# Kernel tuning notes

Hardware: AMD Instinct MI355X
Metric: run time of the kernel (lower is better)

The kernel has to match this reference:

```python
import jax, jax.numpy as jnp
import numpy as np

HEADS = 8
DEPTH = 4
DIM = 128
FF_DIM = 4 * DIM
EPS = 1e-5


def _layer_norm(x, g, b):
    m = jnp.mean(x, axis=-1, keepdims=True)
    v = jnp.mean(jnp.square(x - m), axis=-1, keepdims=True)
    return (x - m) * jax.lax.rsqrt(v + EPS) * g + b


def _linear_attn(x, Wq, Wk, Wv, Wo, bo):
    # lucidrains linear-attention-transformer global (non-causal) linear attention
    b, n, d = x.shape
    dh = d // HEADS
    q = (x @ Wq).reshape(b, n, HEADS, dh).transpose(0, 2, 1, 3)  # bhnd
    k = (x @ Wk).reshape(b, n, HEADS, dh).transpose(0, 2, 1, 3)
    v = (x @ Wv).reshape(b, n, HEADS, dh).transpose(0, 2, 1, 3)
    q = jax.nn.softmax(q, axis=-1) * (dh ** -0.5)  # softmax over feature dim
    k = jax.nn.softmax(k, axis=2)                  # softmax over sequence dim
    ctx = jnp.einsum('bhnd,bhne->bhde', k, v)      # [b,h,dh,dh]
    o = jnp.einsum('bhnd,bhde->bhne', q, ctx)
    o = o.transpose(0, 2, 1, 3).reshape(b, n, d)
    return o @ Wo + bo


def _ff(x, W1, b1, W2, b2):
    return jax.nn.gelu(x @ W1 + b1) @ W2 + b2


def _stack(x, p):
    Wq, Wk, Wv, Wo, bo, g1, be1, g2, be2, W1, bf1, W2, bf2 = p
    for i in range(DEPTH):  # fixed small depth, structurally distinct params
        x = x + _linear_attn(_layer_norm(x, g1[i], be1[i]), Wq[i], Wk[i], Wv[i], Wo[i], bo[i])
        x = x + _ff(_layer_norm(x, g2[i], be2[i]), W1[i], bf1[i], W2[i], bf2[i])
    return x


def _make_stack_params(key):
    ks = jax.random.split(key, 6)
    w = lambda k, s: jax.random.normal(k, s, jnp.float32) * 0.02
    return dict(
        Wq=w(ks[0], (DEPTH, DIM, DIM)), Wk=w(ks[1], (DEPTH, DIM, DIM)),
        Wv=w(ks[2], (DEPTH, DIM, DIM)), Wo=w(ks[3], (DEPTH, DIM, DIM)),
        bo=jnp.zeros((DEPTH, DIM), jnp.float32),
        g1=jnp.ones((DEPTH, DIM), jnp.float32), be1=jnp.zeros((DEPTH, DIM), jnp.float32),
        g2=jnp.ones((DEPTH, DIM), jnp.float32), be2=jnp.zeros((DEPTH, DIM), jnp.float32),
        W1=w(ks[4], (DEPTH, DIM, FF_DIM)), bf1=jnp.zeros((DEPTH, FF_DIM), jnp.float32),
        W2=w(ks[5], (DEPTH, FF_DIM, DIM)), bf2=jnp.zeros((DEPTH, DIM), jnp.float32),
    )


def setup_inputs() -> dict:
    key = jax.random.key(0)
    kx, kc, kt = jax.random.split(key, 3)
    x = jax.random.normal(kx, (64, DIM, 62, 64), jnp.float32)  # [B, emb, num_chan, num_patch]
    pc = {k + '_c': v for k, v in _make_stack_params(kc).items()}
    pt = {k + '_t': v for k, v in _make_stack_params(kt).items()}
    return {'x': x, **pc, **pt}


def reference(x,
              Wq_c, Wk_c, Wv_c, Wo_c, bo_c, g1_c, be1_c, g2_c, be2_c, W1_c, bf1_c, W2_c, bf2_c,
              Wq_t, Wk_t, Wv_t, Wo_t, bo_t, g1_t, be1_t, g2_t, be2_t, W1_t, bf1_t, W2_t, bf2_t):
    b, e, c, p = x.shape
    h = jnp.transpose(x, (0, 3, 2, 1)).reshape(b * p, c, e)  # [B*P, C, E] channel attention
    h = _stack(h, (Wq_c, Wk_c, Wv_c, Wo_c, bo_c, g1_c, be1_c, g2_c, be2_c, W1_c, bf1_c, W2_c, bf2_c)).mean(1)
    h = h.reshape(b, p, e)                                   # [B, P, E] temporal attention
    h = _stack(h, (Wq_t, Wk_t, Wv_t, Wo_t, bo_t, g1_t, be1_t, g2_t, be2_t, W1_t, bf1_t, W2_t, bf2_t)).mean(1)
    return h
```

## Files before the change

### kernel.cpp

```cpp
#include <hip/hip_runtime.h>
#include <stdint.h>

typedef unsigned short u16;
typedef unsigned int   u32;
typedef __attribute__((ext_vector_type(8))) short short8;
typedef __attribute__((ext_vector_type(4))) float f32x4;

#define HEADS  8
#define DH     16
#define DIM    128
#define FFD    512
#define NDEPTH 4
#define NEPS   1e-5f
#define NT     256
#define NTP    256
#define LDA    136

#define U_N    14336
#define BK_OFF 2048
#define KT_OFF 2048
#define VT_OFF 10240

__device__ __forceinline__ float bf2f(u16 u) { return __uint_as_float(((u32)u) << 16); }
__device__ __forceinline__ u16 f2bf(float f) {
    u32 u = __float_as_uint(f);
    u32 r = (u + 0x7FFFu + ((u >> 16) & 1u)) >> 16;
    return (u16)r;
}

template <typename T> struct VT;
template <> struct VT<u16> {
    static __device__ __forceinline__ float ld(const u16* p) { return bf2f(*p); }
    static __device__ __forceinline__ void st(u16* p, float v) { *p = f2bf(v); }
};
template <> struct VT<float> {
    static __device__ __forceinline__ float ld(const float* p) { return *p; }
    static __device__ __forceinline__ void st(float* p, float v) { *p = v; }
};

struct SPv { const void* q[13]; };
struct WTs { const u16 *q, *k, *v, *o, *w1, *w2; };

template <typename T> struct SP {
    const T *bo, *g1, *be1, *g2, *be2, *bf1, *bf2;
    __device__ __forceinline__ SP(const SPv& s) {
        bo = (const T*)s.q[4];  g1 = (const T*)s.q[5];  be1 = (const T*)s.q[6];
        g2 = (const T*)s.q[7];  be2 = (const T*)s.q[8]; bf1 = (const T*)s.q[10];
        bf2 = (const T*)s.q[12];
    }
};

__device__ __forceinline__ void zero_acc(f32x4 acc[4][2]) {
    #pragma unroll
    for (int i = 0; i < 4; ++i)
        #pragma unroll
        for (int j = 0; j < 2; ++j) {
            acc[i][j].x = 0.f; acc[i][j].y = 0.f; acc[i][j].z = 0.f; acc[i][j].w = 0.f;
        }
}

__device__ __forceinline__ void gemm_lds(const u16* Ab, const u16* WT, int Ks,
                                         int nc0, int lane, f32x4 acc[4][2]) {
    const int n = lane & 15, quad = lane >> 4;
    #pragma unroll
    for (int ks = 0; ks < 4; ++ks) {
        short8 b0 = *(const short8*)(WT + (size_t)(nc0 + n) * Ks + ks * 32 + quad * 8);
        short8 b1 = *(const short8*)(WT + (size_t)(nc0 + 16 + n) * Ks + ks * 32 + quad * 8);
        #pragma unroll
        for (int mt = 0; mt < 4; ++mt) {
            short8 a = *(const short8*)(Ab + (mt * 16 + n) * LDA + ks * 32 + quad * 8);
            acc[mt][0] = __builtin_amdgcn_mfma_f32_16x16x32_bf16(a, b0, acc[mt][0], 0, 0, 0);
            acc[mt][1] = __builtin_amdgcn_mfma_f32_16x16x32_bf16(a, b1, acc[mt][1], 0, 0, 0);
        }
    }
}

__device__ __forceinline__ void store_bf16_tile(u16* dst, const f32x4 acc[4][2],
                                                int nc0, int lane) {
    const int c = lane & 15, quad = lane >> 4;
    #pragma unroll
    for (int mt = 0; mt < 4; ++mt)
        #pragma unroll
        for (int nt = 0; nt < 2; ++nt) {
            const float* a = (const float*)&acc[mt][nt];
            #pragma unroll
            for (int r = 0; r < 4; ++r)
                dst[(mt * 16 + quad * 4 + r) * LDA + nc0 + nt * 16 + c] = f2bf(a[r]);
        }
}

template <int MV, typename T>
__device__ __forceinline__ void ln_frag(const f32x4 (&h)[4][2], u16* yb, float* red,
                                        const T* g, const T* be,
                                        int lane, int quad, int nc0, int wn) {
    const int cid = lane & 15;
    const int col0 = nc0 + cid, col1 = col0 + 16;
    #pragma unroll
    for (int mt = 0; mt < 4; ++mt) {
        float s1[4], s2[4];
        #pragma unroll
        for (int r = 0; r < 4; ++r) {
            float a = h[mt][0][r], b = h[mt][1][r];
            s1[r] = a + b;
            s2[r] = fmaf(a, a, b * b);
        }
        #pragma unroll
        for (int m = 1; m <= 8; m <<= 1)
            #pragma unroll
            for (int r = 0; r < 4; ++r) {
                s1[r] += __shfl_xor(s1[r], m, 64);
                s2[r] += __shfl_xor(s2[r], m, 64);
            }
        if (cid == 0) {
            #pragma unroll
            for (int r = 0; r < 4; ++r) {
                const int row = mt * 16 + quad * 4 + r;
                red[row * 8 + wn]     = s1[r];
                red[row * 8 + 4 + wn] = s2[r];
            }
        }
    }
    __syncthreads();
    const float gl0 = VT<T>::ld(g + col0), gl1 = VT<T>::ld(g + col1);
    const float bl0 = VT<T>::ld(be + col0), bl1 = VT<T>::ld(be + col1);
    #pragma unroll
    for (int mt = 0; mt < 4; ++mt)
        #pragma unroll
        for (int r = 0; r < 4; ++r) {
            const int row = mt * 16 + quad * 4 + r;
            float4 p1 = *(const float4*)&red[row * 8];
            float4 p2 = *(const float4*)&red[row * 8 + 4];
            float t1 = (p1.x + p1.y) + (p1.z + p1.w);
            float t2 = (p2.x + p2.y) + (p2.z + p2.w);
            float mean = t1 * (1.0f / 128.0f);
            float var  = fmaxf(t2 * (1.0f / 128.0f) - mean * mean, 0.0f);
            float rstd = rsqrtf(var + NEPS);
            const bool valid = row < MV;
            float o0 = valid ? fmaf((h[mt][0][r] - mean) * rstd, gl0, bl0) : 0.0f;
            float o1 = valid ? fmaf((h[mt][1][r] - mean) * rstd, gl1, bl1) : 0.0f;
            yb[row * LDA + col0] = f2bf(o0);
            yb[row * LDA + col1] = f2bf(o1);
        }
    __syncthreads();
}

template <int MV>
__device__ __forceinline__ void ksoftmax_reg(f32x4 (&acc)[4][2], int lane) {
    const int quad = lane >> 4;
    #pragma unroll
    for (int nt = 0; nt < 2; ++nt) {
        float mx = -1e30f;
        #pragma unroll
        for (int mt = 0; mt < 4; ++mt)
            #pragma unroll
            for (int r = 0; r < 4; ++r) {
                const int lrow = mt * 16 + quad * 4 + r;
                mx = fmaxf(mx, (lrow < MV) ? acc[mt][nt][r] : -1e30f);
            }
        mx = fmaxf(mx, __shfl_xor(mx, 16, 64));
        mx = fmaxf(mx, __shfl_xor(mx, 32, 64));
        float s = 0.0f;
        #pragma unroll
        for (int mt = 0; mt < 4; ++mt)
            #pragma unroll
            for (int r = 0; r < 4; ++r) {
                const int lrow = mt * 16 + quad * 4 + r;
                float e = (lrow < MV) ? __expf(acc[mt][nt][r] - mx) : 0.0f;
                acc[mt][nt][r] = e;
                s += e;
            }
        s += __shfl_xor(s, 16, 64);
        s += __shfl_xor(s, 32, 64);
        const float inv = 1.0f / s;
        #pragma unroll
        for (int mt = 0; mt < 4; ++mt)
            #pragma unroll
            for (int r = 0; r < 4; ++r)
                acc[mt][nt][r] *= inv;
    }
}

__device__ __forceinline__ void qsoftmax_scale(f32x4 (&acc)[4][2], int lane) {
    (void)lane;
    #pragma unroll
    for (int mt = 0; mt < 4; ++mt)
        #pragma unroll
        for (int nt = 0; nt < 2; ++nt)
            #pragma unroll
            for (int r = 0; r < 4; ++r) {
                float v = acc[mt][nt][r];
                float mx = v;
                mx = fmaxf(mx, __shfl_xor(mx, 1, 64));
                mx = fmaxf(mx, __shfl_xor(mx, 2, 64));
                mx = fmaxf(mx, __shfl_xor(mx, 4, 64));
                mx = fmaxf(mx, __shfl_xor(mx, 8, 64));
                float e = __expf(v - mx);
                float s = e;
                s += __shfl_xor(s, 1, 64);
                s += __shfl_xor(s, 2, 64);
                s += __shfl_xor(s, 4, 64);
                s += __shfl_xor(s, 8, 64);
                acc[mt][nt][r] = e * (0.25f / s);
            }
}

__device__ __forceinline__ int swzk(int row, int n) {
    return ((row << 7) | (n << 1)) ^ ((row & 7) << 4);
}
__device__ __forceinline__ int swzb(int row, int n) {
    return ((row << 6) | (n << 1)) ^ ((row & 3) << 4);
}

template <int C>
__device__ __forceinline__ void store_kT_chunk(const f32x4 (&a)[4][2], u16* Th,
                                               int lane, int nc0) {
    const int cid = lane & 15, quad = lane >> 4;
    #pragma unroll
    for (int m = 0; m < 2; ++m)
        #pragma unroll
        for (int nt = 0; nt < 2; ++nt) {
            const int row = nc0 + nt * 16 + cid;
            #pragma unroll
            for (int rr = 0; rr < 2; ++rr) {
                const int n = C * 32 + m * 16 + quad * 4 + rr * 2;
                u32 w = (u32)f2bf(a[C * 2 + m][nt][rr * 2]) |
                        ((u32)f2bf(a[C * 2 + m][nt][rr * 2 + 1]) << 16);
                *(u32*)((char*)Th + swzk(row, n)) = w;
            }
        }
}

template <int C>
__device__ __forceinline__ void store_vT_chunk(const f32x4 (&a)[4][2], u16* Th,
                                               int lane, int nc0) {
    const int cid = lane & 15, quad = lane >> 4;
    #pragma unroll
    for (int m = 0; m < 2; ++m)
        #pragma unroll
        for (int nt = 0; nt < 2; ++nt) {
            const int row = nc0 + nt * 16 + cid;
            #pragma unroll
            for (int rr = 0; rr < 2; ++rr) {
                const int n = m * 16 + quad * 4 + rr * 2;
                u32 w = (u32)f2bf(a[C * 2 + m][nt][rr * 2]) |
                        ((u32)f2bf(a[C * 2 + m][nt][rr * 2 + 1]) << 16);
                *(u32*)((char*)Th + swzb(row, n)) = w;
            }
        }
}

template <int C>
__device__ __forceinline__ void ctx_chunk(const u16* kTs, const u16* vTs,
                                          f32x4 (&ctxacc)[2], int lane, int wn) {
    const int cid = lane & 15, quad = lane >> 4;
    #pragma unroll
    for (int h01 = 0; h01 < 2; ++h01) {
        const int row = (wn * 2 + h01) * 16 + cid;
        short8 a = *(const short8*)((const char*)vTs + swzb(row, quad * 8));
        short8 b = *(const short8*)((const char*)kTs + swzk(row, C * 32 + quad * 8));
        ctxacc[h01] = __builtin_amdgcn_mfma_f32_16x16x32_bf16(a, b, ctxacc[h01], 0, 0, 0);
    }
}

__device__ __forceinline__ void o_mfma(u16* qb, const u16* ctxs, int wn, int lane) {
    const int cid = lane & 15, quad = lane >> 4;
    f32x4 z; z.x = 0.f; z.y = 0.f; z.z = 0.f; z.w = 0.f;
    #pragma unroll
    for (int h01 = 0; h01 < 2; ++h01) {
        const int hd = wn * 2 + h01;
        short8 b = {0, 0, 0, 0, 0, 0, 0, 0};
        if (quad < 2)
            b = *(const short8*)(ctxs + hd * 256 + cid * 16 + quad * 8);
        #pragma unroll
        for (int mt = 0; mt < 4; ++mt) {
            short8 a = *(const short8*)(qb + (mt * 16 + cid) * LDA + hd * DH + (quad & 1) * 8);
            f32x4 o = __builtin_amdgcn_mfma_f32_16x16x32_bf16(a, b, z, 0, 0, 0);
            #pragma unroll
            for (int r = 0; r < 4; ++r)
                qb[(mt * 16 + quad * 4 + r) * LDA + hd * DH + cid] = f2bf(o[r]);
        }
    }
}

__device__ __forceinline__ float gelu_f(float v) {
    float u = 0.7978845608028654f * fmaf(0.044715f * v, v * v, v);
    u = fminf(fmaxf(u, -20.0f), 20.0f);
    float e  = __expf(2.0f * u);
    float th = 1.0f - 2.0f / (e + 1.0f);
    return 0.5f * v * (1.0f + th);
}

template <int MV, typename T>
__device__ __forceinline__ void run_stack(f32x4 (&h)[4][2], u16* yb, u16* U16,
                                          const WTs& wt, const SP<T>& p) {
    const int tid = threadIdx.x;
    const int lane = tid & 63, wn = tid >> 6;
    const int quad = lane >> 4, cid = lane & 15;
    const int nc0 = wn * 32;
    const int col0 = nc0 + cid, col1 = col0 + 16;
    float* red  = (float*)U16;
    u16*   bK   = U16 + BK_OFF;
    u16*   kTs  = U16 + KT_OFF;
    u16*   vTs  = U16 + VT_OFF;
    u16*   ctxs = U16;

    for (int L = 0; L < NDEPTH; ++L) {
        const u16* WqT = wt.q + L * 16384;
        const u16* WkT = wt.k + L * 16384;
        const u16* WvT = wt.v + L * 16384;
        const u16* WoT = wt.o + L * 16384;
        const u16* W1T = wt.w1 + L * 65536;
        const u16* W2T = wt.w2 + L * 65536;

        ln_frag<MV, T>(h, yb, red, p.g1 + L * DIM, p.be1 + L * DIM, lane, quad, nc0, wn);

        f32x4 acc[4][2];
        zero_acc(acc);
        gemm_lds(yb, WkT, DIM, nc0, lane, acc);
        ksoftmax_reg<MV>(acc, lane);
        store_kT_chunk<0>(acc, kTs, lane, nc0);
        store_kT_chunk<1>(acc, kTs, lane, nc0);
        zero_acc(acc);
        gemm_lds(yb, WvT, DIM, nc0, lane, acc);
        f32x4 ctxacc[2];
        #pragma unroll
        for (int i = 0; i < 2; ++i) {
            ctxacc[i].x = 0.f; ctxacc[i].y = 0.f; ctxacc[i].z = 0.f; ctxacc[i].w = 0.f;
        }
        store_vT_chunk<0>(acc, vTs, lane, nc0);
        ctx_chunk<0>(kTs, vTs, ctxacc, lane, wn);
        store_vT_chunk<1>(acc, vTs, lane, nc0);
        ctx_chunk<1>(kTs, vTs, ctxacc, lane, wn);
        #pragma unroll
        for (int h01 = 0; h01 < 2; ++h01)
            #pragma unroll
            for (int r = 0; r < 4; ++r)
                ctxs[(wn * 2 + h01) * 256 + (quad * 4 + r) * 16 + cid] = f2bf(ctxacc[h01][r]);

        zero_acc(acc);
        gemm_lds(yb, WqT, DIM, nc0, lane, acc);
        qsoftmax_scale(acc, lane);
        __syncthreads();
        store_bf16_tile(bK, acc, nc0, lane);
        o_mfma(bK, ctxs, wn, lane);
        __syncthreads();

        gemm_lds(bK, WoT, DIM, nc0, lane, h);
        {
            const float b0 = VT<T>::ld(p.bo + L * DIM + col0);
            const float b1 = VT<T>::ld(p.bo + L * DIM + col1);
            #pragma unroll
            for (int mt = 0; mt < 4; ++mt)
                #pragma unroll
                for (int r = 0; r < 4; ++r) { h[mt][0][r] += b0; h[mt][1][r] += b1; }
        }

        ln_frag<MV, T>(h, yb, red, p.g2 + L * DIM, p.be2 + L * DIM, lane, quad, nc0, wn);

        for (int cc = 0; cc < 4; ++cc) {
            zero_acc(acc);
            gemm_lds(yb, W1T + cc * 128 * DIM, DIM, nc0, lane, acc);
            const float b10 = VT<T>::ld(p.bf1 + L * FFD + cc * 128 + col0);
            const float b11 = VT<T>::ld(p.bf1 + L * FFD + cc * 128 + col1);
            #pragma unroll
            for (int mt = 0; mt < 4; ++mt)
                #pragma unroll
                for (int r = 0; r < 4; ++r) {
                    const int row = mt * 16 + quad * 4 + r;
                    bK[row * LDA + col0] = f2bf(gelu_f(acc[mt][0][r] + b10));
                    bK[row * LDA + col1] = f2bf(gelu_f(acc[mt][1][r] + b11));
                }
            __syncthreads();
            gemm_lds(bK, W2T + cc * 128, FFD, nc0, lane, h);
            if (cc < 3) __syncthreads();
        }
        {
            const float b0 = VT<T>::ld(p.bf2 + L * DIM + col0);
            const float b1 = VT<T>::ld(p.bf2 + L * DIM + col1);
            #pragma unroll
            for (int mt = 0; mt < 4; ++mt)
                #pragma unroll
                for (int r = 0; r < 4; ++r) { h[mt][0][r] += b0; h[mt][1][r] += b1; }
        }
    }
}

__device__ __forceinline__ bool is_bf16_g(const void* g1) {
    return *reinterpret_cast<const u32*>(g1) == 0x3F803F80u;
}

template <typename T>
__device__ __forceinline__ void channel_body(const T* x, const float* xT, int xmode,
                                             const SPv& pv, const WTs& wt,
                                             float* pooled, u16* yb, u16* U16) {
    SP<T> p(pv);
    const int tid = threadIdx.x;
    const int lane = tid & 63, wn = tid >> 6;
    const int quad = lane >> 4, cid = lane & 15;
    const int nc0 = wn * 32;
    const int col0 = nc0 + cid, col1 = col0 + 16;
    const int seq = blockIdx.x;

    f32x4 h[4][2];
    if (xmode) {
        const float* xrow = xT + (size_t)seq * 62 * DIM;
        #pragma unroll
        for (int mt = 0; mt < 4; ++mt)
            #pragma unroll
            for (int r = 0; r < 4; ++r) {
                const int row = mt * 16 + quad * 4 + r;
                h[mt][0][r] = (row < 62) ? xrow[row * DIM + col0] : 0.0f;
                h[mt][1][r] = (row < 62) ? xrow[row * DIM + col1] : 0.0f;
            }
    } else {
        const int b = seq >> 6, pp = seq & 63;
        #pragma unroll
        for (int mt = 0; mt < 4; ++mt)
            #pragma unroll
            for (int r = 0; r < 4; ++r) {
                const int row = mt * 16 + quad * 4 + r;
                h[mt][0][r] = (row < 62)
                    ? VT<T>::ld(x + (((size_t)b * DIM + col0) * 62 + row) * 64 + pp) : 0.0f;
                h[mt][1][r] = (row < 62)
                    ? VT<T>::ld(x + (((size_t)b * DIM + col1) * 62 + row) * 64 + pp) : 0.0f;
            }
    }

    run_stack<62, T>(h, yb, U16, wt, p);

    float s0 = 0.0f, s1 = 0.0f;
    #pragma unroll
    for (int mt = 0; mt < 4; ++mt)
        #pragma unroll
        for (int r = 0; r < 4; ++r) {
            const int row = mt * 16 + quad * 4 + r;
            if (row < 62) { s0 += h[mt][0][r]; s1 += h[mt][1][r]; }
        }
    s0 += __shfl_xor(s0, 16, 64); s0 += __shfl_xor(s0, 32, 64);
    s1 += __shfl_xor(s1, 16, 64); s1 += __shfl_xor(s1, 32, 64);
    if (quad == 0) {
        pooled[(size_t)seq * DIM + col0] = s0 * (1.0f / 62.0f);
        pooled[(size_t)seq * DIM + col1] = s1 * (1.0f / 62.0f);
    }
}

template <typename T>
__device__ __forceinline__ void temporal_body(const float* pooled, const SPv& pv,
                                              const WTs& wt, T* out, u16* yb, u16* U16) {
    SP<T> p(pv);
    const int tid = threadIdx.x;
    const int lane = tid & 63, wn = tid >> 6;
    const int quad = lane >> 4, cid = lane & 15;
    const int nc0 = wn * 32;
    const int col0 = nc0 + cid, col1 = col0 + 16;
    const int seq = blockIdx.x;

    f32x4 h[4][2];
    #pragma unroll
    for (int mt = 0; mt < 4; ++mt)
        #pragma unroll
        for (int r = 0; r < 4; ++r) {
            const int row = mt * 16 + quad * 4 + r;
            h[mt][0][r] = pooled[((size_t)seq * 64 + row) * DIM + col0];
            h[mt][1][r] = pooled[((size_t)seq * 64 + row) * DIM + col1];
        }

    run_stack<64, T>(h, yb, U16, wt, p);

    float s0 = 0.0f, s1 = 0.0f;
    #pragma unroll
    for (int mt = 0; mt < 4; ++mt)
        #pragma unroll
        for (int r = 0; r < 4; ++r) { s0 += h[mt][0][r]; s1 += h[mt][1][r]; }
    s0 += __shfl_xor(s0, 16, 64); s0 += __shfl_xor(s0, 32, 64);
    s1 += __shfl_xor(s1, 16, 64); s1 += __shfl_xor(s1, 32, 64);
    if (quad == 0) {
        VT<T>::st(out + (size_t)seq * DIM + col0, s0 * (1.0f / 64.0f));
        VT<T>::st(out + (size_t)seq * DIM + col1, s1 * (1.0f / 64.0f));
    }
}

__global__ __launch_bounds__(NT, 2) void k_channel(const void* xv, const float* xT,
                                                   int xmode, SPv pv, WTs wt,
                                                   float* __restrict__ pooled) {
    __shared__ __attribute__((aligned(16))) u16 yb[64 * LDA];
    __shared__ __attribute__((aligned(16))) u16 Ubuf[U_N];

    if (is_bf16_g(pv.q[5]))
        channel_body<u16>((const u16*)xv, xT, xmode, pv, wt, pooled, yb, Ubuf);
    else
        channel_body<float>((const float*)xv, xT, xmode, pv, wt, pooled, yb, Ubuf);
}

__global__ __launch_bounds__(NT, 2) void k_temporal(const float* __restrict__ pooled,
                                                    SPv pv, WTs wt, void* outv) {
    __shared__ __attribute__((aligned(16))) u16 yb[64 * LDA];
    __shared__ __attribute__((aligned(16))) u16 Ubuf[U_N];

    if (is_bf16_g(pv.q[5]))
        temporal_body<u16>(pooled, pv, wt, (u16*)outv, yb, Ubuf);
    else
        temporal_body<float>(pooled, pv, wt, (float*)outv, yb, Ubuf);
}

template <typename T>
__device__ __forceinline__ void prepx_body(const T* x, float* xT, float* t) {
    const int tid = threadIdx.x;
    const int b = blockIdx.x >> 3, cg = blockIdx.x & 7;
    const int c1 = (cg == 7) ? 62 : (cg * 8 + 8);
    for (int c = cg * 8; c < c1; ++c) {
        #pragma unroll 4
        for (int rep = 0; rep < 32; ++rep) {
            const int idx = rep * NTP + tid;
            const int e = idx >> 6, pp = idx & 63;
            t[pp * 132 + e] = VT<T>::ld(x + (((size_t)b * DIM + e) * 62 + c) * 64 + pp);
        }
        __syncthreads();
        #pragma unroll 4
        for (int rep = 0; rep < 32; ++rep) {
            const int idx = rep * NTP + tid;
            const int pp = idx >> 7, e = idx & 127;
            xT[((size_t)(b * 64 + pp) * 62 + c) * DIM + e] = t[pp * 132 + e];
        }
        __syncthreads();
    }
}

__global__ __launch_bounds__(NTP) void k_prepx(const void* xv, const void* g1, float* xT) {
    __shared__ float t[64 * 132];
    if (is_bf16_g(g1)) prepx_body<u16>((const u16*)xv, xT, t);
    else               prepx_body<float>((const float*)xv, xT, t);
}

struct TD { const void* src; u16* dst; int K; int N; int nelem; };
struct TDs { TD a[12]; const void* g1; };

__global__ __launch_bounds__(NTP) void k_prep(TDs t) {
    const bool bf = (*(const u32*)t.g1 == 0x3F803F80u);
    int idx = blockIdx.x * NTP + threadIdx.x;
    #pragma unroll 1
    for (int i = 0; i < 12; ++i) {
        if (idx < t.a[i].nelem) {
            const int K = t.a[i].K, N = t.a[i].N;
            const int l = idx / (K * N);
            const int r = idx - l * K * N;
            const int n = r / K;
            const int k = r - n * K;
            const size_t si = ((size_t)l * K + k) * N + n;
            float v = bf ? bf2f(((const u16*)t.a[i].src)[si])
                         : ((const float*)t.a[i].src)[si];
            t.a[i].dst[idx] = f2bf(v);
            return;
        }
        idx -= t.a[i].nelem;
    }
}

extern "C" void kernel_launch(void* const* d_in, const int* in_sizes, int n_in,
                              void* d_out, int out_size, void* d_ws, size_t ws_size,
                              hipStream_t stream) {
    (void)in_sizes; (void)n_in; (void)out_size;
    SPv pc, pt;
    for (int i = 0; i < 13; ++i) pc.q[i] = d_in[1 + i];
    for (int i = 0; i < 13; ++i) pt.q[i] = d_in[14 + i];

    float* pooled = (float*)d_ws;
    u16*   wtb    = (u16*)((char*)d_ws + (size_t)4096 * 128 * 4);
    const size_t XT_OFF = 8u << 20;
    float* xT     = (float*)((char*)d_ws + XT_OFF);
    const size_t xt_need = XT_OFF + (size_t)4096 * 62 * DIM * 4;
    const int xmode = (ws_size >= xt_need) ? 1 : 0;

    const int SQ = 4 * DIM * DIM;
    const int SF = 4 * DIM * FFD;
    const int STK = 4 * SQ + 2 * SF;

    WTs wc { wtb, wtb + SQ, wtb + 2 * SQ, wtb + 3 * SQ, wtb + 4 * SQ, wtb + 4 * SQ + SF };
    u16* wtb2 = wtb + STK;
    WTs wt2 { wtb2, wtb2 + SQ, wtb2 + 2 * SQ, wtb2 + 3 * SQ, wtb2 + 4 * SQ, wtb2 + 4 * SQ + SF };

    TDs td;
    td.a[0]  = { d_in[1],  (u16*)wc.q,  DIM, DIM, SQ };
    td.a[1]  = { d_in[2],  (u16*)wc.k,  DIM, DIM, SQ };
    td.a[2]  = { d_in[3],  (u16*)wc.v,  DIM, DIM, SQ };
    td.a[3]  = { d_in[4],  (u16*)wc.o,  DIM, DIM, SQ };
    td.a[4]  = { d_in[10], (u16*)wc.w1, DIM, FFD, SF };
    td.a[5]  = { d_in[12], (u16*)wc.w2, FFD, DIM, SF };
    td.a[6]  = { d_in[14], (u16*)wt2.q,  DIM, DIM, SQ };
    td.a[7]  = { d_in[15], (u16*)wt2.k,  DIM, DIM, SQ };
    td.a[8]  = { d_in[16], (u16*)wt2.v,  DIM, DIM, SQ };
    td.a[9]  = { d_in[17], (u16*)wt2.o,  DIM, DIM, SQ };
    td.a[10] = { d_in[23], (u16*)wt2.w1, DIM, FFD, SF };
    td.a[11] = { d_in[25], (u16*)wt2.w2, FFD, DIM, SF };
    td.g1 = d_in[6];

    const int total = 2 * STK;
    k_prep<<<dim3((total + NTP - 1) / NTP), dim3(NTP), 0, stream>>>(td);
    if (xmode)
        k_prepx<<<dim3(64 * 8), dim3(NTP), 0, stream>>>(d_in[0], d_in[6], xT);

    k_channel<<<dim3(4096), dim3(NT), 0, stream>>>(d_in[0], xT, xmode, pc, wc, pooled);
    k_temporal<<<dim3(64),  dim3(NT), 0, stream>>>(pooled, pt, wt2, d_out);
}
```

Measured before the change: 2.038 ms.

## Use 8 waves per block with one head per wave instead of 4 waves

Blocks grow from 256 to 512 threads, so each wave owns 16 output columns (one attention head) instead of 32. The GEMM, softmax, LayerNorm reduction and context computation are reworked so each wave handles one head, with per-wave transposed K/V scratch and a wider cross-wave reduction buffer. This aims to raise the number of active waves and cut per-thread register pressure. In exchange each B-fragment load feeds fewer MFMAs, shared memory per block grows, and barriers now synchronise twice as many waves.

```diff
diff --git a/kernel.cpp b/kernel.cpp
--- a/kernel.cpp
+++ b/kernel.cpp
@@ -12,11 +12,11 @@
 #define FFD    512
 #define NDEPTH 4
 #define NEPS   1e-5f
-#define NT     256
+#define NT     512
 #define NTP    256
 #define LDA    136
 
-#define U_N    14336
+#define U_N    18432
 #define BK_OFF 2048
 #define KT_OFF 2048
 #define VT_OFF 10240
@@ -50,59 +50,50 @@
     }
 };
 
-__device__ __forceinline__ void zero_acc(f32x4 acc[4][2]) {
-    #pragma unroll
-    for (int i = 0; i < 4; ++i)
-        #pragma unroll
-        for (int j = 0; j < 2; ++j) {
-            acc[i][j].x = 0.f; acc[i][j].y = 0.f; acc[i][j].z = 0.f; acc[i][j].w = 0.f;
-        }
+__device__ __forceinline__ void zero4(f32x4 acc[4]) {
+    #pragma unroll
+    for (int i = 0; i < 4; ++i) {
+        acc[i].x = 0.f; acc[i].y = 0.f; acc[i].z = 0.f; acc[i].w = 0.f;
+    }
 }
 
 __device__ __forceinline__ void gemm_lds(const u16* Ab, const u16* WT, int Ks,
-                                         int nc0, int lane, f32x4 acc[4][2]) {
+                                         int nc0, int lane, f32x4 acc[4]) {
     const int n = lane & 15, quad = lane >> 4;
     #pragma unroll
     for (int ks = 0; ks < 4; ++ks) {
         short8 b0 = *(const short8*)(WT + (size_t)(nc0 + n) * Ks + ks * 32 + quad * 8);
-        short8 b1 = *(const short8*)(WT + (size_t)(nc0 + 16 + n) * Ks + ks * 32 + quad * 8);
         #pragma unroll
         for (int mt = 0; mt < 4; ++mt) {
             short8 a = *(const short8*)(Ab + (mt * 16 + n) * LDA + ks * 32 + quad * 8);
-            acc[mt][0] = __builtin_amdgcn_mfma_f32_16x16x32_bf16(a, b0, acc[mt][0], 0, 0, 0);
-            acc[mt][1] = __builtin_amdgcn_mfma_f32_16x16x32_bf16(a, b1, acc[mt][1], 0, 0, 0);
-        }
-    }
-}
-
-__device__ __forceinline__ void store_bf16_tile(u16* dst, const f32x4 acc[4][2],
+            acc[mt] = __builtin_amdgcn_mfma_f32_16x16x32_bf16(a, b0, acc[mt], 0, 0, 0);
+        }
+    }
+}
+
+__device__ __forceinline__ void store_bf16_tile(u16* dst, const f32x4 acc[4],
                                                 int nc0, int lane) {
     const int c = lane & 15, quad = lane >> 4;
     #pragma unroll
     for (int mt = 0; mt < 4; ++mt)
         #pragma unroll
-        for (int nt = 0; nt < 2; ++nt) {
-            const float* a = (const float*)&acc[mt][nt];
-            #pragma unroll
-            for (int r = 0; r < 4; ++r)
-                dst[(mt * 16 + quad * 4 + r) * LDA + nc0 + nt * 16 + c] = f2bf(a[r]);
-        }
+        for (int r = 0; r < 4; ++r)
+            dst[(mt * 16 + quad * 4 + r) * LDA + nc0 + c] = f2bf(acc[mt][r]);
 }
 
 template <int MV, typename T>
-__device__ __forceinline__ void ln_frag(const f32x4 (&h)[4][2], u16* yb, float* red,
+__device__ __forceinline__ void ln_frag(const f32x4 (&h)[4], u16* yb, float* red,
                                         const T* g, const T* be,
-                                        int lane, int quad, int nc0, int wn) {
+                                        int lane, int quad, int col0, int wn) {
     const int cid = lane & 15;
-    const int col0 = nc0 + cid, col1 = col0 + 16;
     #pragma unroll
     for (int mt = 0; mt < 4; ++mt) {
         float s1[4], s2[4];
         #pragma unroll
         for (int r = 0; r < 4; ++r) {
-            float a = h[mt][0][r], b = h[mt][1][r];
-            s1[r] = a + b;
-            s2[r] = fmaf(a, a, b * b);
+            float a = h[mt][r];
+            s1[r] = a;
+            s2[r] = a * a;
         }
         #pragma unroll
         for (int m = 1; m <= 8; m <<= 1)
@@ -115,170 +106,127 @@
             #pragma unroll
             for (int r = 0; r < 4; ++r) {
                 const int row = mt * 16 + quad * 4 + r;
-                red[row * 8 + wn]     = s1[r];
-                red[row * 8 + 4 + wn] = s2[r];
+                red[row * 16 + wn]     = s1[r];
+                red[row * 16 + 8 + wn] = s2[r];
             }
         }
     }
     __syncthreads();
-    const float gl0 = VT<T>::ld(g + col0), gl1 = VT<T>::ld(g + col1);
-    const float bl0 = VT<T>::ld(be + col0), bl1 = VT<T>::ld(be + col1);
+    const float gl0 = VT<T>::ld(g + col0);
+    const float bl0 = VT<T>::ld(be + col0);
     #pragma unroll
     for (int mt = 0; mt < 4; ++mt)
         #pragma unroll
         for (int r = 0; r < 4; ++r) {
             const int row = mt * 16 + quad * 4 + r;
-            float4 p1 = *(const float4*)&red[row * 8];
-            float4 p2 = *(const float4*)&red[row * 8 + 4];
-            float t1 = (p1.x + p1.y) + (p1.z + p1.w);
-            float t2 = (p2.x + p2.y) + (p2.z + p2.w);
+            float4 a1 = *(const float4*)&red[row * 16];
+            float4 b1 = *(const float4*)&red[row * 16 + 4];
+            float4 a2 = *(const float4*)&red[row * 16 + 8];
+            float4 b2 = *(const float4*)&red[row * 16 + 12];
+            float t1 = ((a1.x + a1.y) + (a1.z + a1.w)) + ((b1.x + b1.y) + (b1.z + b1.w));
+            float t2 = ((a2.x + a2.y) + (a2.z + a2.w)) + ((b2.x + b2.y) + (b2.z + b2.w));
             float mean = t1 * (1.0f / 128.0f);
             float var  = fmaxf(t2 * (1.0f / 128.0f) - mean * mean, 0.0f);
             float rstd = rsqrtf(var + NEPS);
             const bool valid = row < MV;
-            float o0 = valid ? fmaf((h[mt][0][r] - mean) * rstd, gl0, bl0) : 0.0f;
-            float o1 = valid ? fmaf((h[mt][1][r] - mean) * rstd, gl1, bl1) : 0.0f;
+            float o0 = valid ? fmaf((h[mt][r] - mean) * rstd, gl0, bl0) : 0.0f;
             yb[row * LDA + col0] = f2bf(o0);
-            yb[row * LDA + col1] = f2bf(o1);
         }
     __syncthreads();
 }
 
 template <int MV>
-__device__ __forceinline__ void ksoftmax_reg(f32x4 (&acc)[4][2], int lane) {
+__device__ __forceinline__ void ksoftmax_reg(f32x4 (&acc)[4], int lane) {
     const int quad = lane >> 4;
-    #pragma unroll
-    for (int nt = 0; nt < 2; ++nt) {
-        float mx = -1e30f;
-        #pragma unroll
-        for (int mt = 0; mt < 4; ++mt)
-            #pragma unroll
-            for (int r = 0; r < 4; ++r) {
-                const int lrow = mt * 16 + quad * 4 + r;
-                mx = fmaxf(mx, (lrow < MV) ? acc[mt][nt][r] : -1e30f);
-            }
-        mx = fmaxf(mx, __shfl_xor(mx, 16, 64));
-        mx = fmaxf(mx, __shfl_xor(mx, 32, 64));
-        float s = 0.0f;
-        #pragma unroll
-        for (int mt = 0; mt < 4; ++mt)
-            #pragma unroll
-            for (int r = 0; r < 4; ++r) {
-                const int lrow = mt * 16 + quad * 4 + r;
-                float e = (lrow < MV) ? __expf(acc[mt][nt][r] - mx) : 0.0f;
-                acc[mt][nt][r] = e;
-                s += e;
-            }
-        s += __shfl_xor(s, 16, 64);
-        s += __shfl_xor(s, 32, 64);
-        const float inv = 1.0f / s;
-        #pragma unroll
-        for (int mt = 0; mt < 4; ++mt)
-            #pragma unroll
-            for (int r = 0; r < 4; ++r)
-                acc[mt][nt][r] *= inv;
-    }
-}
-
-__device__ __forceinline__ void qsoftmax_scale(f32x4 (&acc)[4][2], int lane) {
-    (void)lane;
-    #pragma unroll
-    for (int mt = 0; mt < 4; ++mt)
-        #pragma unroll
-        for (int nt = 0; nt < 2; ++nt)
-            #pragma unroll
-            for (int r = 0; r < 4; ++r) {
-                float v = acc[mt][nt][r];
-                float mx = v;
-                mx = fmaxf(mx, __shfl_xor(mx, 1, 64));
-                mx = fmaxf(mx, __shfl_xor(mx, 2, 64));
-                mx = fmaxf(mx, __shfl_xor(mx, 4, 64));
-                mx = fmaxf(mx, __shfl_xor(mx, 8, 64));
-                float e = __expf(v - mx);
-                float s = e;
-                s += __shfl_xor(s, 1, 64);
-                s += __shfl_xor(s, 2, 64);
-                s += __shfl_xor(s, 4, 64);
-                s += __shfl_xor(s, 8, 64);
-                acc[mt][nt][r] = e * (0.25f / s);
-            }
-}
-
-__device__ __forceinline__ int swzk(int row, int n) {
-    return ((row << 7) | (n << 1)) ^ ((row & 7) << 4);
-}
-__device__ __forceinline__ int swzb(int row, int n) {
-    return ((row << 6) | (n << 1)) ^ ((row & 3) << 4);
-}
-
-template <int C>
-__device__ __forceinline__ void store_kT_chunk(const f32x4 (&a)[4][2], u16* Th,
-                                               int lane, int nc0) {
+    float mx = -1e30f;
+    #pragma unroll
+    for (int mt = 0; mt < 4; ++mt)
+        #pragma unroll
+        for (int r = 0; r < 4; ++r) {
+            const int lrow = mt * 16 + quad * 4 + r;
+            mx = fmaxf(mx, (lrow < MV) ? acc[mt][r] : -1e30f);
+        }
+    mx = fmaxf(mx, __shfl_xor(mx, 16, 64));
+    mx = fmaxf(mx, __shfl_xor(mx, 32, 64));
+    float s = 0.0f;
+    #pragma unroll
+    for (int mt = 0; mt < 4; ++mt)
+        #pragma unroll
+        for (int r = 0; r < 4; ++r) {
+            const int lrow = mt * 16 + quad * 4 + r;
+            float e = (lrow < MV) ? __expf(acc[mt][r] - mx) : 0.0f;
+            acc[mt][r] = e;
+            s += e;
+        }
+    s += __shfl_xor(s, 16, 64);
+    s += __shfl_xor(s, 32, 64);
+    const float inv = 1.0f / s;
+    #pragma unroll
+    for (int mt = 0; mt < 4; ++mt)
+        #pragma unroll
+        for (int r = 0; r < 4; ++r)
+            acc[mt][r] *= inv;
+}
+
+__device__ __forceinline__ void qsoftmax_scale(f32x4 (&acc)[4]) {
+    #pragma unroll
+    for (int mt = 0; mt < 4; ++mt)
+        #pragma unroll
+        for (int r = 0; r < 4; ++r) {
+            float v = acc[mt][r];
+            float mx = v;
+            mx = fmaxf(mx, __shfl_xor(mx, 1, 64));
+            mx = fmaxf(mx, __shfl_xor(mx, 2, 64));
+            mx = fmaxf(mx, __shfl_xor(mx, 4, 64));
+            mx = fmaxf(mx, __shfl_xor(mx, 8, 64));
+            float e = __expf(v - mx);
+            float s = e;
+            s += __shfl_xor(s, 1, 64);
+            s += __shfl_xor(s, 2, 64);
+            s += __shfl_xor(s, 4, 64);
+            s += __shfl_xor(s, 8, 64);
+            acc[mt][r] = e * (0.25f / s);
+        }
+}
+
+__device__ __forceinline__ void store_T16(const f32x4 (&a)[4], u16* Tw, int lane) {
     const int cid = lane & 15, quad = lane >> 4;
     #pragma unroll
-    for (int m = 0; m < 2; ++m)
-        #pragma unroll
-        for (int nt = 0; nt < 2; ++nt) {
-            const int row = nc0 + nt * 16 + cid;
-            #pragma unroll
-            for (int rr = 0; rr < 2; ++rr) {
-                const int n = C * 32 + m * 16 + quad * 4 + rr * 2;
-                u32 w = (u32)f2bf(a[C * 2 + m][nt][rr * 2]) |
-                        ((u32)f2bf(a[C * 2 + m][nt][rr * 2 + 1]) << 16);
-                *(u32*)((char*)Th + swzk(row, n)) = w;
-            }
-        }
-}
-
-template <int C>
-__device__ __forceinline__ void store_vT_chunk(const f32x4 (&a)[4][2], u16* Th,
-                                               int lane, int nc0) {
+    for (int mt = 0; mt < 4; ++mt)
+        #pragma unroll
+        for (int rr = 0; rr < 2; ++rr) {
+            const int n = mt * 16 + quad * 4 + rr * 2;
+            u32 w = (u32)f2bf(a[mt][rr * 2]) | ((u32)f2bf(a[mt][rr * 2 + 1]) << 16);
+            int off = ((cid << 7) + (n << 1)) ^ ((cid & 7) << 4);
+            *(u32*)((char*)Tw + off) = w;
+        }
+}
+
+__device__ __forceinline__ void ctx16(const u16* kTw, const u16* vTw,
+                                      f32x4& ctxacc, int lane) {
     const int cid = lane & 15, quad = lane >> 4;
     #pragma unroll
-    for (int m = 0; m < 2; ++m)
-        #pragma unroll
-        for (int nt = 0; nt < 2; ++nt) {
-            const int row = nc0 + nt * 16 + cid;
-            #pragma unroll
-            for (int rr = 0; rr < 2; ++rr) {
-                const int n = m * 16 + quad * 4 + rr * 2;
-                u32 w = (u32)f2bf(a[C * 2 + m][nt][rr * 2]) |
-                        ((u32)f2bf(a[C * 2 + m][nt][rr * 2 + 1]) << 16);
-                *(u32*)((char*)Th + swzb(row, n)) = w;
-            }
-        }
-}
-
-template <int C>
-__device__ __forceinline__ void ctx_chunk(const u16* kTs, const u16* vTs,
-                                          f32x4 (&ctxacc)[2], int lane, int wn) {
-    const int cid = lane & 15, quad = lane >> 4;
-    #pragma unroll
-    for (int h01 = 0; h01 < 2; ++h01) {
-        const int row = (wn * 2 + h01) * 16 + cid;
-        short8 a = *(const short8*)((const char*)vTs + swzb(row, quad * 8));
-        short8 b = *(const short8*)((const char*)kTs + swzk(row, C * 32 + quad * 8));
-        ctxacc[h01] = __builtin_amdgcn_mfma_f32_16x16x32_bf16(a, b, ctxacc[h01], 0, 0, 0);
-    }
-}
-
-__device__ __forceinline__ void o_mfma(u16* qb, const u16* ctxs, int wn, int lane) {
+    for (int ks = 0; ks < 2; ++ks) {
+        int off = ((cid << 7) + ks * 64 + quad * 16) ^ ((cid & 7) << 4);
+        short8 a = *(const short8*)((const char*)vTw + off);
+        short8 b = *(const short8*)((const char*)kTw + off);
+        ctxacc = __builtin_amdgcn_mfma_f32_16x16x32_bf16(a, b, ctxacc, 0, 0, 0);
+    }
+}
+
+__device__ __forceinline__ void o_mfma16(u16* qb, const u16* ctxs, int wn, int lane) {
     const int cid = lane & 15, quad = lane >> 4;
     f32x4 z; z.x = 0.f; z.y = 0.f; z.z = 0.f; z.w = 0.f;
-    #pragma unroll
-    for (int h01 = 0; h01 < 2; ++h01) {
-        const int hd = wn * 2 + h01;
-        short8 b = {0, 0, 0, 0, 0, 0, 0, 0};
-        if (quad < 2)
-            b = *(const short8*)(ctxs + hd * 256 + cid * 16 + quad * 8);
-        #pragma unroll
-        for (int mt = 0; mt < 4; ++mt) {
-            short8 a = *(const short8*)(qb + (mt * 16 + cid) * LDA + hd * DH + (quad & 1) * 8);
-            f32x4 o = __builtin_amdgcn_mfma_f32_16x16x32_bf16(a, b, z, 0, 0, 0);
-            #pragma unroll
-            for (int r = 0; r < 4; ++r)
-                qb[(mt * 16 + quad * 4 + r) * LDA + hd * DH + cid] = f2bf(o[r]);
-        }
+    short8 b = {0, 0, 0, 0, 0, 0, 0, 0};
+    if (quad < 2)
+        b = *(const short8*)(ctxs + wn * 256 + cid * 16 + quad * 8);
+    #pragma unroll
+    for (int mt = 0; mt < 4; ++mt) {
+        short8 a = *(const short8*)(qb + (mt * 16 + cid) * LDA + wn * 16 + (quad & 1) * 8);
+        f32x4 o = __builtin_amdgcn_mfma_f32_16x16x32_bf16(a, b, z, 0, 0, 0);
+        #pragma unroll
+        for (int r = 0; r < 4; ++r)
+            qb[(mt * 16 + quad * 4 + r) * LDA + wn * 16 + cid] = f2bf(o[r]);
     }
 }
 
@@ -291,18 +239,18 @@
 }
 
 template <int MV, typename T>
-__device__ __forceinline__ void run_stack(f32x4 (&h)[4][2], u16* yb, u16* U16,
+__device__ __forceinline__ void run_stack(f32x4 (&h)[4], u16* yb, u16* U16,
                                           const WTs& wt, const SP<T>& p) {
     const int tid = threadIdx.x;
     const int lane = tid & 63, wn = tid >> 6;
     const int quad = lane >> 4, cid = lane & 15;
-    const int nc0 = wn * 32;
-    const int col0 = nc0 + cid, col1 = col0 + 16;
+    const int nc0 = wn * 16;
+    const int col0 = nc0 + cid;
     float* red  = (float*)U16;
+    u16*   ctxs = U16;
     u16*   bK   = U16 + BK_OFF;
-    u16*   kTs  = U16 + KT_OFF;
-    u16*   vTs  = U16 + VT_OFF;
-    u16*   ctxs = U16;
+    u16*   kTw  = U16 + KT_OFF + wn * 1024;
+    u16*   vTw  = U16 + VT_OFF + wn * 1024;
 
     for (int L = 0; L < NDEPTH; ++L) {
         const u16* WqT = wt.q + L * 16384;
@@ -312,63 +260,51 @@
         const u16* W1T = wt.w1 + L * 65536;
         const u16* W2T = wt.w2 + L * 65536;
 
-        ln_frag<MV, T>(h, yb, red, p.g1 + L * DIM, p.be1 + L * DIM, lane, quad, nc0, wn);
-
-        f32x4 acc[4][2];
-        zero_acc(acc);
+        ln_frag<MV, T>(h, yb, red, p.g1 + L * DIM, p.be1 + L * DIM, lane, quad, col0, wn);
+
+        f32x4 acc[4];
+        zero4(acc);
         gemm_lds(yb, WkT, DIM, nc0, lane, acc);
         ksoftmax_reg<MV>(acc, lane);
-        store_kT_chunk<0>(acc, kTs, lane, nc0);
-        store_kT_chunk<1>(acc, kTs, lane, nc0);
-        zero_acc(acc);
+        store_T16(acc, kTw, lane);
+        zero4(acc);
         gemm_lds(yb, WvT, DIM, nc0, lane, acc);
-        f32x4 ctxacc[2];
-        #pragma unroll
-        for (int i = 0; i < 2; ++i) {
-            ctxacc[i].x = 0.f; ctxacc[i].y = 0.f; ctxacc[i].z = 0.f; ctxacc[i].w = 0.f;
-        }
-        store_vT_chunk<0>(acc, vTs, lane, nc0);
-        ctx_chunk<0>(kTs, vTs, ctxacc, lane, wn);
-        store_vT_chunk<1>(acc, vTs, lane, nc0);
-        ctx_chunk<1>(kTs, vTs, ctxacc, lane, wn);
-        #pragma unroll
-        for (int h01 = 0; h01 < 2; ++h01)
-            #pragma unroll
-            for (int r = 0; r < 4; ++r)
-                ctxs[(wn * 2 + h01) * 256 + (quad * 4 + r) * 16 + cid] = f2bf(ctxacc[h01][r]);
-
-        zero_acc(acc);
+        store_T16(acc, vTw, lane);
+        f32x4 ctxacc; ctxacc.x = 0.f; ctxacc.y = 0.f; ctxacc.z = 0.f; ctxacc.w = 0.f;
+        ctx16(kTw, vTw, ctxacc, lane);
+        #pragma unroll
+        for (int r = 0; r < 4; ++r)
+            ctxs[wn * 256 + (quad * 4 + r) * 16 + cid] = f2bf(ctxacc[r]);
+
+        zero4(acc);
         gemm_lds(yb, WqT, DIM, nc0, lane, acc);
-        qsoftmax_scale(acc, lane);
+        qsoftmax_scale(acc);
         __syncthreads();
         store_bf16_tile(bK, acc, nc0, lane);
-        o_mfma(bK, ctxs, wn, lane);
+        o_mfma16(bK, ctxs, wn, lane);
         __syncthreads();
 
         gemm_lds(bK, WoT, DIM, nc0, lane, h);
         {
             const float b0 = VT<T>::ld(p.bo + L * DIM + col0);
-            const float b1 = VT<T>::ld(p.bo + L * DIM + col1);
             #pragma unroll
             for (int mt = 0; mt < 4; ++mt)
                 #pragma unroll
-                for (int r = 0; r < 4; ++r) { h[mt][0][r] += b0; h[mt][1][r] += b1; }
-        }
-
-        ln_frag<MV, T>(h, yb, red, p.g2 + L * DIM, p.be2 + L * DIM, lane, quad, nc0, wn);
+                for (int r = 0; r < 4; ++r) h[mt][r] += b0;
+        }
+
+        ln_frag<MV, T>(h, yb, red, p.g2 + L * DIM, p.be2 + L * DIM, lane, quad, col0, wn);
 
         for (int cc = 0; cc < 4; ++cc) {
-            zero_acc(acc);
+            zero4(acc);
             gemm_lds(yb, W1T + cc * 128 * DIM, DIM, nc0, lane, acc);
             const float b10 = VT<T>::ld(p.bf1 + L * FFD + cc * 128 + col0);
-            const float b11 = VT<T>::ld(p.bf1 + L * FFD + cc * 128 + col1);
             #pragma unroll
             for (int mt = 0; mt < 4; ++mt)
                 #pragma unroll
                 for (int r = 0; r < 4; ++r) {
                     const int row = mt * 16 + quad * 4 + r;
-                    bK[row * LDA + col0] = f2bf(gelu_f(acc[mt][0][r] + b10));
-                    bK[row * LDA + col1] = f2bf(gelu_f(acc[mt][1][r] + b11));
+                    bK[row * LDA + col0] = f2bf(gelu_f(acc[mt][r] + b10));
                 }
             __syncthreads();
             gemm_lds(bK, W2T + cc * 128, FFD, nc0, lane, h);
@@ -376,11 +312,10 @@
         }
         {
             const float b0 = VT<T>::ld(p.bf2 + L * DIM + col0);
-            const float b1 = VT<T>::ld(p.bf2 + L * DIM + col1);
             #pragma unroll
             for (int mt = 0; mt < 4; ++mt)
                 #pragma unroll
-                for (int r = 0; r < 4; ++r) { h[mt][0][r] += b0; h[mt][1][r] += b1; }
+                for (int r = 0; r < 4; ++r) h[mt][r] += b0;
         }
     }
 }
@@ -397,11 +332,10 @@
     const int tid = threadIdx.x;
     const int lane = tid & 63, wn = tid >> 6;
     const int quad = lane >> 4, cid = lane & 15;
-    const int nc0 = wn * 32;
-    const int col0 = nc0 + cid, col1 = col0 + 16;
+    const int col0 = wn * 16 + cid;
     const int seq = blockIdx.x;
 
-    f32x4 h[4][2];
+    f32x4 h[4];
     if (xmode) {
         const float* xrow = xT + (size_t)seq * 62 * DIM;
         #pragma unroll
@@ -409,8 +343,7 @@
             #pragma unroll
             for (int r = 0; r < 4; ++r) {
                 const int row = mt * 16 + quad * 4 + r;
-                h[mt][0][r] = (row < 62) ? xrow[row * DIM + col0] : 0.0f;
-                h[mt][1][r] = (row < 62) ? xrow[row * DIM + col1] : 0.0f;
+                h[mt][r] = (row < 62) ? xrow[row * DIM + col0] : 0.0f;
             }
     } else {
         const int b = seq >> 6, pp = seq & 63;
@@ -419,29 +352,24 @@
             #pragma unroll
             for (int r = 0; r < 4; ++r) {
                 const int row = mt * 16 + quad * 4 + r;
-                h[mt][0][r] = (row < 62)
+                h[mt][r] = (row < 62)
                     ? VT<T>::ld(x + (((size_t)b * DIM + col0) * 62 + row) * 64 + pp) : 0.0f;
-                h[mt][1][r] = (row < 62)
-                    ? VT<T>::ld(x + (((size_t)b * DIM + col1) * 62 + row) * 64 + pp) : 0.0f;
             }
     }
 
     run_stack<62, T>(h, yb, U16, wt, p);
 
-    float s0 = 0.0f, s1 = 0.0f;
+    float s0 = 0.0f;
     #pragma unroll
     for (int mt = 0; mt < 4; ++mt)
         #pragma unroll
         for (int r = 0; r < 4; ++r) {
             const int row = mt * 16 + quad * 4 + r;
-            if (row < 62) { s0 += h[mt][0][r]; s1 += h[mt][1][r]; }
+            if (row < 62) s0 += h[mt][r];
         }
     s0 += __shfl_xor(s0, 16, 64); s0 += __shfl_xor(s0, 32, 64);
-    s1 += __shfl_xor(s1, 16, 64); s1 += __shfl_xor(s1, 32, 64);
-    if (quad == 0) {
+    if (quad == 0)
         pooled[(size_t)seq * DIM + col0] = s0 * (1.0f / 62.0f);
-        pooled[(size_t)seq * DIM + col1] = s1 * (1.0f / 62.0f);
-    }
 }
 
 template <typename T>
@@ -451,36 +379,31 @@
     const int tid = threadIdx.x;
     const int lane = tid & 63, wn = tid >> 6;
     const int quad = lane >> 4, cid = lane & 15;
-    const int nc0 = wn * 32;
-    const int col0 = nc0 + cid, col1 = col0 + 16;
+    const int col0 = wn * 16 + cid;
     const int seq = blockIdx.x;
 
-    f32x4 h[4][2];
+    f32x4 h[4];
     #pragma unroll
     for (int mt = 0; mt < 4; ++mt)
         #pragma unroll
         for (int r = 0; r < 4; ++r) {
             const int row = mt * 16 + quad * 4 + r;
-            h[mt][0][r] = pooled[((size_t)seq * 64 + row) * DIM + col0];
-            h[mt][1][r] = pooled[((size_t)seq * 64 + row) * DIM + col1];
+            h[mt][r] = pooled[((size_t)seq * 64 + row) * DIM + col0];
         }
 
     run_stack<64, T>(h, yb, U16, wt, p);
 
-    float s0 = 0.0f, s1 = 0.0f;
-    #pragma unroll
-    for (int mt = 0; mt < 4; ++mt)
-        #pragma unroll
-        for (int r = 0; r < 4; ++r) { s0 += h[mt][0][r]; s1 += h[mt][1][r]; }
+    float s0 = 0.0f;
+    #pragma unroll
+    for (int mt = 0; mt < 4; ++mt)
+        #pragma unroll
+        for (int r = 0; r < 4; ++r) s0 += h[mt][r];
     s0 += __shfl_xor(s0, 16, 64); s0 += __shfl_xor(s0, 32, 64);
-    s1 += __shfl_xor(s1, 16, 64); s1 += __shfl_xor(s1, 32, 64);
-    if (quad == 0) {
+    if (quad == 0)
         VT<T>::st(out + (size_t)seq * DIM + col0, s0 * (1.0f / 64.0f));
-        VT<T>::st(out + (size_t)seq * DIM + col1, s1 * (1.0f / 64.0f));
-    }
-}
-
-__global__ __launch_bounds__(NT, 2) void k_channel(const void* xv, const float* xT,
+}
+
+__global__ __launch_bounds__(NT, 4) void k_channel(const void* xv, const float* xT,
                                                    int xmode, SPv pv, WTs wt,
                                                    float* __restrict__ pooled) {
     __shared__ __attribute__((aligned(16))) u16 yb[64 * LDA];
@@ -492,7 +415,7 @@
         channel_body<float>((const float*)xv, xT, xmode, pv, wt, pooled, yb, Ubuf);
 }
 
-__global__ __launch_bounds__(NT, 2) void k_temporal(const float* __restrict__ pooled,
+__global__ __launch_bounds__(NT, 4) void k_temporal(const float* __restrict__ pooled,
                                                     SPv pv, WTs wt, void* outv) {
     __shared__ __attribute__((aligned(16))) u16 yb[64 * LDA];
     __shared__ __attribute__((aligned(16))) u16 Ubuf[U_N];
```

Result: slower. 2.589 ms (+27.1%).

## Double-buffer FF hidden chunks in LDS and use fast reciprocals in softmax/GELU

Applied to the files above, without the earlier changes.

The feed-forward loop now ping-pongs between two LDS buffers. The next chunk's W1 GEMM and GELU are computed while the current chunk feeds the W2 GEMM, which removes one barrier per chunk. Divisions in the key softmax, query softmax and GELU are replaced with the hardware approximate reciprocal. The query softmax also drops its max-subtraction, which saves four shuffles per element but risks overflow for large logits. The LDS footprint grows by about 17 KB, which may lower occupancy.

```diff
diff --git a/kernel.cpp b/kernel.cpp
--- a/kernel.cpp
+++ b/kernel.cpp
@@ -16,10 +16,11 @@
 #define NTP    256
 #define LDA    136
 
-#define U_N    14336
-#define BK_OFF 2048
-#define KT_OFF 2048
-#define VT_OFF 10240
+#define U_N     23040
+#define BK_OFF  2048
+#define KT_OFF  2048
+#define VT_OFF  10240
+#define BK2_OFF 14336
 
 __device__ __forceinline__ float bf2f(u16 u) { return __uint_as_float(((u32)u) << 16); }
 __device__ __forceinline__ u16 f2bf(float f) {
@@ -171,7 +172,7 @@
             }
         s += __shfl_xor(s, 16, 64);
         s += __shfl_xor(s, 32, 64);
-        const float inv = 1.0f / s;
+        const float inv = __builtin_amdgcn_rcpf(s);
         #pragma unroll
         for (int mt = 0; mt < 4; ++mt)
             #pragma unroll
@@ -188,19 +189,13 @@
         for (int nt = 0; nt < 2; ++nt)
             #pragma unroll
             for (int r = 0; r < 4; ++r) {
-                float v = acc[mt][nt][r];
-                float mx = v;
-                mx = fmaxf(mx, __shfl_xor(mx, 1, 64));
-                mx = fmaxf(mx, __shfl_xor(mx, 2, 64));
-                mx = fmaxf(mx, __shfl_xor(mx, 4, 64));
-                mx = fmaxf(mx, __shfl_xor(mx, 8, 64));
-                float e = __expf(v - mx);
+                float e = __expf(acc[mt][nt][r]);
                 float s = e;
                 s += __shfl_xor(s, 1, 64);
                 s += __shfl_xor(s, 2, 64);
                 s += __shfl_xor(s, 4, 64);
                 s += __shfl_xor(s, 8, 64);
-                acc[mt][nt][r] = e * (0.25f / s);
+                acc[mt][nt][r] = e * (0.25f * __builtin_amdgcn_rcpf(s));
             }
 }
 
@@ -286,8 +281,24 @@
     float u = 0.7978845608028654f * fmaf(0.044715f * v, v * v, v);
     u = fminf(fmaxf(u, -20.0f), 20.0f);
     float e  = __expf(2.0f * u);
-    float th = 1.0f - 2.0f / (e + 1.0f);
+    float th = 1.0f - 2.0f * __builtin_amdgcn_rcpf(e + 1.0f);
     return 0.5f * v * (1.0f + th);
+}
+
+template <typename T>
+__device__ __forceinline__ void gelu_store(const f32x4 (&acc)[4][2], u16* dst,
+                                           const T* bf1, int col0, int col1,
+                                           int quad) {
+    const float b10 = VT<T>::ld(bf1 + col0);
+    const float b11 = VT<T>::ld(bf1 + col1);
+    #pragma unroll
+    for (int mt = 0; mt < 4; ++mt)
+        #pragma unroll
+        for (int r = 0; r < 4; ++r) {
+            const int row = mt * 16 + quad * 4 + r;
+            dst[row * LDA + col0] = f2bf(gelu_f(acc[mt][0][r] + b10));
+            dst[row * LDA + col1] = f2bf(gelu_f(acc[mt][1][r] + b11));
+        }
 }
 
 template <int MV, typename T>
@@ -299,7 +310,8 @@
     const int nc0 = wn * 32;
     const int col0 = nc0 + cid, col1 = col0 + 16;
     float* red  = (float*)U16;
-    u16*   bK   = U16 + BK_OFF;
+    u16*   bKa  = U16 + BK_OFF;
+    u16*   bKb  = U16 + BK2_OFF;
     u16*   kTs  = U16 + KT_OFF;
     u16*   vTs  = U16 + VT_OFF;
     u16*   ctxs = U16;
@@ -341,11 +353,11 @@
         gemm_lds(yb, WqT, DIM, nc0, lane, acc);
         qsoftmax_scale(acc, lane);
         __syncthreads();
-        store_bf16_tile(bK, acc, nc0, lane);
-        o_mfma(bK, ctxs, wn, lane);
+        store_bf16_tile(bKa, acc, nc0, lane);
+        o_mfma(bKa, ctxs, wn, lane);
         __syncthreads();
 
-        gemm_lds(bK, WoT, DIM, nc0, lane, h);
+        gemm_lds(bKa, WoT, DIM, nc0, lane, h);
         {
             const float b0 = VT<T>::ld(p.bo + L * DIM + col0);
             const float b1 = VT<T>::ld(p.bo + L * DIM + col1);
@@ -357,22 +369,23 @@
 
         ln_frag<MV, T>(h, yb, red, p.g2 + L * DIM, p.be2 + L * DIM, lane, quad, nc0, wn);
 
+        zero_acc(acc);
+        gemm_lds(yb, W1T, DIM, nc0, lane, acc);
+        gelu_store(acc, bKa, p.bf1 + L * FFD, col0, col1, quad);
+        __syncthreads();
+        #pragma unroll
         for (int cc = 0; cc < 4; ++cc) {
-            zero_acc(acc);
-            gemm_lds(yb, W1T + cc * 128 * DIM, DIM, nc0, lane, acc);
-            const float b10 = VT<T>::ld(p.bf1 + L * FFD + cc * 128 + col0);
-            const float b11 = VT<T>::ld(p.bf1 + L * FFD + cc * 128 + col1);
-            #pragma unroll
-            for (int mt = 0; mt < 4; ++mt)
-                #pragma unroll
-                for (int r = 0; r < 4; ++r) {
-                    const int row = mt * 16 + quad * 4 + r;
-                    bK[row * LDA + col0] = f2bf(gelu_f(acc[mt][0][r] + b10));
-                    bK[row * LDA + col1] = f2bf(gelu_f(acc[mt][1][r] + b11));
-                }
-            __syncthreads();
-            gemm_lds(bK, W2T + cc * 128, FFD, nc0, lane, h);
-            if (cc < 3) __syncthreads();
+            u16* cur = (cc & 1) ? bKb : bKa;
+            u16* nxt = (cc & 1) ? bKa : bKb;
+            if (cc < 3) {
+                zero_acc(acc);
+                gemm_lds(yb, W1T + (cc + 1) * 128 * DIM, DIM, nc0, lane, acc);
+            }
+            gemm_lds(cur, W2T + cc * 128, FFD, nc0, lane, h);
+            if (cc < 3) {
+                gelu_store(acc, nxt, p.bf1 + L * FFD + (cc + 1) * 128, col0, col1, quad);
+                __syncthreads();
+            }
         }
         {
             const float b0 = VT<T>::ld(p.bf2 + L * DIM + col0);
```

Measured after the change: 1.718 ms. 1.19x faster.
